# Optimization experiments

Measured on AMD Instinct MI355X. Metric: run time of the kernel, lower is better.

Reference implementation:

```python
import jax, jax.numpy as jnp
import numpy as np

NUM_LAYERS = 3
HIDDEN = 64
NUM_CLASSES = 4096
LN_EPS = 1e-5


def setup_inputs() -> dict:
    key = jax.random.key(0)
    ks = jax.random.split(key, 8)
    B, N, E, H = 8, NUM_CLASSES, 131072, HIDDEN
    node_features = jax.random.normal(ks[0], (B, N, H), dtype=jnp.float32)
    edge_indices = jax.random.randint(ks[1], (B, 2, E), 0, N, dtype=jnp.int64)
    edge_attrs = jax.random.normal(ks[2], (B, E, H), dtype=jnp.float32)
    # GraphConvolutionLayer params (xavier_uniform weight, zero bias) per layer
    limit = np.sqrt(6.0 / (H + H)).astype(np.float32)
    W = jax.random.uniform(ks[3], (NUM_LAYERS, H, H), minval=-limit, maxval=limit, dtype=jnp.float32)
    b = jnp.zeros((NUM_LAYERS, H), dtype=jnp.float32)
    gamma = jnp.ones((NUM_LAYERS, H), dtype=jnp.float32)
    beta = jnp.zeros((NUM_LAYERS, H), dtype=jnp.float32)
    global_emb = 0.02 * jax.random.normal(ks[4], (N, H), dtype=jnp.float32)
    return {
        "node_features": node_features,
        "edge_indices": edge_indices,
        "edge_attrs": edge_attrs,
        "W": W,
        "b": b,
        "gamma": gamma,
        "beta": beta,
        "global_emb": global_emb,
    }


def _layer_norm(x, g, bt):
    mu = jnp.mean(x, axis=-1, keepdims=True)
    var = jnp.mean((x - mu) ** 2, axis=-1, keepdims=True)
    return (x - mu) * jax.lax.rsqrt(var + LN_EPS) * g + bt


def reference(node_features, edge_indices, edge_attrs, W, b, gamma, beta, global_emb):
    N = node_features.shape[1]

    def per_graph(x0, ei, ea):
        # presence mask computed on raw node features [N, 1]
        presence = (jnp.sum(x0, axis=1) != 0).astype(x0.dtype)[:, None]
        src, dst = ei[0], ei[1]
        x = x0
        for i in range(NUM_LAYERS):
            residual = x
            h = x @ W[i]                                   # [N, H]
            msg = h[src] * ea                              # gather + edge gate [E, H]
            out = jax.ops.segment_sum(msg, dst, num_segments=N) + b[i]
            out = jax.nn.relu(out)
            out = _layer_norm(out, gamma[i], beta[i])
            x = out + residual if i > 0 else out
        return x * presence + global_emb * (1.0 - presence)

    return jax.vmap(per_graph)(node_features, edge_indices, edge_attrs)
```

## Files before the change

kernel.cpp:

```cpp
#include <hip/hip_runtime.h>

#define GB 8
#define GN 4096
#define GH 64
#define GE 131072
#define LN_EPS 1e-5f
#define NBIN (GB * GN)
#define TOTE (GB * GE)

static __device__ __forceinline__ unsigned short f2bf(float f) {
    union { float f; unsigned int u; } v; v.f = f;
    unsigned int u = v.u;
    return (unsigned short)((u + 0x7FFFu + ((u >> 16) & 1u)) >> 16);
}
static __device__ __forceinline__ void bf2x(unsigned int u, float& lo, float& hi) {
    union { float f; unsigned int i; } a, b;
    a.i = u << 16; b.i = u & 0xFFFF0000u;
    lo = a.f; hi = b.f;
}
static __device__ __forceinline__ void fma8(uint4 ev, uint4 hv, float4& a0, float4& a1) {
    float el, eh, hl, hh;
    bf2x(ev.x, el, eh); bf2x(hv.x, hl, hh);
    a0.x = fmaf(el, hl, a0.x); a0.y = fmaf(eh, hh, a0.y);
    bf2x(ev.y, el, eh); bf2x(hv.y, hl, hh);
    a0.z = fmaf(el, hl, a0.z); a0.w = fmaf(eh, hh, a0.w);
    bf2x(ev.z, el, eh); bf2x(hv.z, hl, hh);
    a1.x = fmaf(el, hl, a1.x); a1.y = fmaf(eh, hh, a1.y);
    bf2x(ev.w, el, eh); bf2x(hv.w, hl, hh);
    a1.z = fmaf(el, hl, a1.z); a1.w = fmaf(eh, hh, a1.w);
}

__global__ void k_init(const float* __restrict__ nf, float* __restrict__ pres) {
    int w = (blockIdx.x * blockDim.x + threadIdx.x) >> 6;
    int lane = threadIdx.x & 63;
    if (w >= NBIN) return;
    float v = nf[(size_t)w * GH + lane];
    #pragma unroll
    for (int o = 1; o < 64; o <<= 1) v += __shfl_xor(v, o, 64);
    if (lane == 0) pres[w] = (v != 0.0f) ? 1.0f : 0.0f;
}

__global__ void k_hist(const int* __restrict__ ei, int* __restrict__ hist) {
    int t = blockIdx.x * blockDim.x + threadIdx.x;
    int b = t >> 17, e = t & (GE - 1);
    int dst = ei[(b << 18) + GE + e];
    atomicAdd(&hist[(b << 12) + dst], 1);
}

__global__ void k_scan(const int* __restrict__ hist, int* __restrict__ off,
                       int* __restrict__ cur) {
    __shared__ int part[256];
    int b = blockIdx.x;
    int t = threadIdx.x;
    int base = (b << 12) + t * 16;
    int c[16];
    int s = 0;
    #pragma unroll
    for (int i = 0; i < 16; ++i) { c[i] = hist[base + i]; s += c[i]; }
    part[t] = s;
    __syncthreads();
    for (int o = 1; o < 256; o <<= 1) {
        int u = (t >= o) ? part[t - o] : 0;
        __syncthreads();
        part[t] += u;
        __syncthreads();
    }
    int p = b * GE + part[t] - s;
    #pragma unroll
    for (int i = 0; i < 16; ++i) { off[base + i] = p; cur[base + i] = p; p += c[i]; }
    if (b == GB - 1 && t == 255) off[NBIN] = TOTE;
}

__global__ void k_fillperm(const int* __restrict__ ei, int* __restrict__ cur,
                           const float* __restrict__ ea,
                           int* __restrict__ sSrc, unsigned short* __restrict__ ea_s) {
    int grp = (blockIdx.x * blockDim.x + threadIdx.x) >> 4;
    if (grp >= TOTE) return;
    int sub  = threadIdx.x & 15;
    int lane = threadIdx.x & 63;
    int b = grp >> 17, e = grp & (GE - 1);
    int dst = ei[(b << 18) + GE + e];
    int pos = 0;
    if (sub == 0) pos = atomicAdd(&cur[(b << 12) + dst], 1);
    pos = __shfl(pos, lane & ~15, 64);
    float4 v = *reinterpret_cast<const float4*>(ea + ((size_t)grp << 6) + (sub << 2));
    ushort4 o;
    o.x = f2bf(v.x); o.y = f2bf(v.y); o.z = f2bf(v.z); o.w = f2bf(v.w);
    *reinterpret_cast<ushort4*>(ea_s + ((size_t)pos << 6) + (sub << 2)) = o;
    if (sub == 0) sSrc[pos] = ei[(b << 18) + e];
}

__global__ void k_gemm(const float* __restrict__ x, const float* __restrict__ W,
                       unsigned short* __restrict__ h, int layer) {
    __shared__ float Wl[GH * GH];
    for (int i = threadIdx.x; i < GH * GH; i += blockDim.x)
        Wl[i] = W[layer * GH * GH + i];
    __syncthreads();
    int w = (blockIdx.x * blockDim.x + threadIdx.x) >> 6;
    int lane = threadIdx.x & 63;
    if (w >= NBIN) return;
    float xv = x[(size_t)w * GH + lane];
    float acc = 0.0f;
    #pragma unroll
    for (int k = 0; k < GH; ++k)
        acc = fmaf(__shfl(xv, k, 64), Wl[k * GH + lane], acc);
    h[(size_t)w * GH + lane] = f2bf(acc);
}

__global__ void k_gather(const int* __restrict__ off, const int* __restrict__ sSrc,
                         const unsigned short* __restrict__ ea_s,
                         const unsigned short* __restrict__ h,
                         const float* __restrict__ bias, const float* __restrict__ gam,
                         const float* __restrict__ bet,
                         float* __restrict__ x, const float* __restrict__ pres,
                         const float* __restrict__ ge, float* __restrict__ out,
                         int layer) {
    int w = (blockIdx.x * blockDim.x + threadIdx.x) >> 6;
    if (w >= NBIN) return;
    int lane = threadIdx.x & 63;
    int g   = lane >> 3;
    int sub = lane & 7;
    int b = w >> 12;
    int beg = off[w], end = off[w + 1];
    const unsigned short* hb = h + ((((size_t)b) << 12) * GH);

    float4 a0 = make_float4(0.f, 0.f, 0.f, 0.f);
    float4 a1 = make_float4(0.f, 0.f, 0.f, 0.f);
    for (int e = beg; e < end; e += 16) {
        int e0 = e + g;
        int e1 = e + 8 + g;
        if (e0 < end) {
            int s0 = sSrc[e0];
            uint4 ev = *reinterpret_cast<const uint4*>(ea_s + (((size_t)e0) << 6) + (sub << 3));
            uint4 hv = *reinterpret_cast<const uint4*>(hb + (((size_t)s0) << 6) + (sub << 3));
            fma8(ev, hv, a0, a1);
        }
        if (e1 < end) {
            int s1 = sSrc[e1];
            uint4 ev = *reinterpret_cast<const uint4*>(ea_s + (((size_t)e1) << 6) + (sub << 3));
            uint4 hv = *reinterpret_cast<const uint4*>(hb + (((size_t)s1) << 6) + (sub << 3));
            fma8(ev, hv, a0, a1);
        }
    }
    #pragma unroll
    for (int o = 8; o < 64; o <<= 1) {
        a0.x += __shfl_xor(a0.x, o, 64);
        a0.y += __shfl_xor(a0.y, o, 64);
        a0.z += __shfl_xor(a0.z, o, 64);
        a0.w += __shfl_xor(a0.w, o, 64);
        a1.x += __shfl_xor(a1.x, o, 64);
        a1.y += __shfl_xor(a1.y, o, 64);
        a1.z += __shfl_xor(a1.z, o, 64);
        a1.w += __shfl_xor(a1.w, o, 64);
    }

    const float4* bias4 = reinterpret_cast<const float4*>(bias + layer * GH + (sub << 3));
    float4 b0 = bias4[0], b1 = bias4[1];
    float4 v0, v1;
    v0.x = fmaxf(a0.x + b0.x, 0.f); v0.y = fmaxf(a0.y + b0.y, 0.f);
    v0.z = fmaxf(a0.z + b0.z, 0.f); v0.w = fmaxf(a0.w + b0.w, 0.f);
    v1.x = fmaxf(a1.x + b1.x, 0.f); v1.y = fmaxf(a1.y + b1.y, 0.f);
    v1.z = fmaxf(a1.z + b1.z, 0.f); v1.w = fmaxf(a1.w + b1.w, 0.f);
    float s = v0.x + v0.y + v0.z + v0.w + v1.x + v1.y + v1.z + v1.w;
    #pragma unroll
    for (int o = 1; o < 8; o <<= 1) s += __shfl_xor(s, o, 64);
    float mu = s * (1.0f / GH);
    float4 d0, d1;
    d0.x = v0.x - mu; d0.y = v0.y - mu; d0.z = v0.z - mu; d0.w = v0.w - mu;
    d1.x = v1.x - mu; d1.y = v1.y - mu; d1.z = v1.z - mu; d1.w = v1.w - mu;
    float q = d0.x*d0.x + d0.y*d0.y + d0.z*d0.z + d0.w*d0.w
            + d1.x*d1.x + d1.y*d1.y + d1.z*d1.z + d1.w*d1.w;
    #pragma unroll
    for (int o = 1; o < 8; o <<= 1) q += __shfl_xor(q, o, 64);
    float r = rsqrtf(q * (1.0f / GH) + LN_EPS);
    const float4* gam4 = reinterpret_cast<const float4*>(gam + layer * GH + (sub << 3));
    const float4* bet4 = reinterpret_cast<const float4*>(bet + layer * GH + (sub << 3));
    float4 g0 = gam4[0], g1 = gam4[1];
    float4 t0 = bet4[0], t1 = bet4[1];
    float4 y0, y1;
    y0.x = d0.x * r * g0.x + t0.x; y0.y = d0.y * r * g0.y + t0.y;
    y0.z = d0.z * r * g0.z + t0.z; y0.w = d0.w * r * g0.w + t0.w;
    y1.x = d1.x * r * g1.x + t1.x; y1.y = d1.y * r * g1.y + t1.y;
    y1.z = d1.z * r * g1.z + t1.z; y1.w = d1.w * r * g1.w + t1.w;

    if (g == 0) {
        float4* xp = reinterpret_cast<float4*>(x + (size_t)w * GH + (sub << 3));
        if (layer > 0) {
            float4 x0 = xp[0], x1 = xp[1];
            y0.x += x0.x; y0.y += x0.y; y0.z += x0.z; y0.w += x0.w;
            y1.x += x1.x; y1.y += x1.y; y1.z += x1.z; y1.w += x1.w;
        }
        if (layer < 2) {
            xp[0] = y0; xp[1] = y1;
        } else {
            float p = pres[w];
            const float4* ge4 = reinterpret_cast<const float4*>(ge + (size_t)(w & (GN - 1)) * GH + (sub << 3));
            float4 e0 = ge4[0], e1 = ge4[1];
            float4 o0, o1;
            o0.x = y0.x * p + e0.x * (1.f - p); o0.y = y0.y * p + e0.y * (1.f - p);
            o0.z = y0.z * p + e0.z * (1.f - p); o0.w = y0.w * p + e0.w * (1.f - p);
            o1.x = y1.x * p + e1.x * (1.f - p); o1.y = y1.y * p + e1.y * (1.f - p);
            o1.z = y1.z * p + e1.z * (1.f - p); o1.w = y1.w * p + e1.w * (1.f - p);
            float4* op = reinterpret_cast<float4*>(out + (size_t)w * GH + (sub << 3));
            op[0] = o0; op[1] = o1;
        }
    }
}

extern "C" void kernel_launch(void* const* d_in, const int* in_sizes, int n_in,
                              void* d_out, int out_size, void* d_ws, size_t ws_size,
                              hipStream_t stream) {
    const float* nf = (const float*)d_in[0];
    const int* ei   = (const int*)d_in[1];
    const float* ea = (const float*)d_in[2];
    const float* W  = (const float*)d_in[3];
    const float* bb = (const float*)d_in[4];
    const float* gg = (const float*)d_in[5];
    const float* be = (const float*)d_in[6];
    const float* ge = (const float*)d_in[7];
    float* out = (float*)d_out;

    float* x    = (float*)d_ws;
    float* pres = x + (size_t)NBIN * GH;
    int* off    = (int*)(pres + NBIN);
    int* cur    = off + NBIN + 1;
    int* hist   = cur + NBIN;
    int* sSrc   = hist + NBIN;
    unsigned short* h_s  = (unsigned short*)(sSrc + TOTE);
    unsigned short* ea_s = h_s + (size_t)NBIN * GH;

    hipMemsetAsync(hist, 0, NBIN * sizeof(int), stream);
    k_init<<<NBIN / 4, 256, 0, stream>>>(nf, pres);
    k_hist<<<TOTE / 256, 256, 0, stream>>>(ei, hist);
    k_scan<<<GB, 256, 0, stream>>>(hist, off, cur);
    k_fillperm<<<TOTE / 16, 256, 0, stream>>>(ei, cur, ea, sSrc, ea_s);

    for (int l = 0; l < 3; ++l) {
        k_gemm<<<NBIN / 4, 256, 0, stream>>>(l == 0 ? nf : x, W, h_s, l);
        k_gather<<<NBIN / 4, 256, 0, stream>>>(off, sSrc, ea_s, h_s, bb, gg, be,
                                               x, pres, ge, out, l);
    }
}
```

Measured before the change: 403.6 us.

## Sort edges by destination within fixed windows instead of per graph

Splits each graph's edge list into eight windows and builds a counting-sort by destination inside each window, so the permutation scatter of edge attributes stays within a smaller memory region. The scan runs over 64 windows instead of 8 graphs. The gather kernel now walks eight short per-window segments per node, which adds offset loads and shorter, less-filled inner loops in a kernel that runs once per layer.

```diff
diff --git a/kernel.cpp b/kernel.cpp
--- a/kernel.cpp
+++ b/kernel.cpp
@@ -7,6 +7,8 @@
 #define LN_EPS 1e-5f
 #define NBIN (GB * GN)
 #define TOTE (GB * GE)
+#define NWIN 64
+#define WSZ  (TOTE / NWIN)
 
 static __device__ __forceinline__ unsigned short f2bf(float f) {
     union { float f; unsigned int u; } v; v.f = f;
@@ -40,23 +42,24 @@
     if (lane == 0) pres[w] = (v != 0.0f) ? 1.0f : 0.0f;
 }
 
-__global__ void k_hist(const int* __restrict__ ei, int* __restrict__ hist) {
+__global__ void k_hist2(const int* __restrict__ ei, int* __restrict__ hist2) {
     int t = blockIdx.x * blockDim.x + threadIdx.x;
     int b = t >> 17, e = t & (GE - 1);
     int dst = ei[(b << 18) + GE + e];
-    atomicAdd(&hist[(b << 12) + dst], 1);
-}
-
-__global__ void k_scan(const int* __restrict__ hist, int* __restrict__ off,
-                       int* __restrict__ cur) {
+    int w = t >> 14;
+    atomicAdd(&hist2[(w << 12) + dst], 1);
+}
+
+__global__ void k_scan2(const int* __restrict__ hist2, int* __restrict__ off2,
+                        int* __restrict__ cur2) {
     __shared__ int part[256];
-    int b = blockIdx.x;
+    int w = blockIdx.x;
     int t = threadIdx.x;
-    int base = (b << 12) + t * 16;
+    int base = (w << 12) + t * 16;
     int c[16];
     int s = 0;
     #pragma unroll
-    for (int i = 0; i < 16; ++i) { c[i] = hist[base + i]; s += c[i]; }
+    for (int i = 0; i < 16; ++i) { c[i] = hist2[base + i]; s += c[i]; }
     part[t] = s;
     __syncthreads();
     for (int o = 1; o < 256; o <<= 1) {
@@ -65,23 +68,23 @@
         part[t] += u;
         __syncthreads();
     }
-    int p = b * GE + part[t] - s;
-    #pragma unroll
-    for (int i = 0; i < 16; ++i) { off[base + i] = p; cur[base + i] = p; p += c[i]; }
-    if (b == GB - 1 && t == 255) off[NBIN] = TOTE;
-}
-
-__global__ void k_fillperm(const int* __restrict__ ei, int* __restrict__ cur,
-                           const float* __restrict__ ea,
-                           int* __restrict__ sSrc, unsigned short* __restrict__ ea_s) {
+    int p = (w << 14) + part[t] - s;
+    #pragma unroll
+    for (int i = 0; i < 16; ++i) { off2[base + i] = p; cur2[base + i] = p; p += c[i]; }
+}
+
+__global__ void k_wperm(const int* __restrict__ ei, int* __restrict__ cur2,
+                        const float* __restrict__ ea,
+                        int* __restrict__ sSrc, unsigned short* __restrict__ ea_s) {
     int grp = (blockIdx.x * blockDim.x + threadIdx.x) >> 4;
     if (grp >= TOTE) return;
     int sub  = threadIdx.x & 15;
     int lane = threadIdx.x & 63;
     int b = grp >> 17, e = grp & (GE - 1);
+    int w = grp >> 14;
     int dst = ei[(b << 18) + GE + e];
     int pos = 0;
-    if (sub == 0) pos = atomicAdd(&cur[(b << 12) + dst], 1);
+    if (sub == 0) pos = atomicAdd(&cur2[(w << 12) + dst], 1);
     pos = __shfl(pos, lane & ~15, 64);
     float4 v = *reinterpret_cast<const float4*>(ea + ((size_t)grp << 6) + (sub << 2));
     ushort4 o;
@@ -107,7 +110,7 @@
     h[(size_t)w * GH + lane] = f2bf(acc);
 }
 
-__global__ void k_gather(const int* __restrict__ off, const int* __restrict__ sSrc,
+__global__ void k_gather(const int* __restrict__ off2, const int* __restrict__ sSrc,
                          const unsigned short* __restrict__ ea_s,
                          const unsigned short* __restrict__ h,
                          const float* __restrict__ bias, const float* __restrict__ gam,
@@ -120,26 +123,25 @@
     int lane = threadIdx.x & 63;
     int g   = lane >> 3;
     int sub = lane & 7;
-    int b = w >> 12;
-    int beg = off[w], end = off[w + 1];
-    const unsigned short* hb = h + ((((size_t)b) << 12) * GH);
+    int grf = w >> 12;
+    int dst = w & (GN - 1);
+    const unsigned short* hb = h + ((((size_t)grf) << 12) * GH);
 
     float4 a0 = make_float4(0.f, 0.f, 0.f, 0.f);
     float4 a1 = make_float4(0.f, 0.f, 0.f, 0.f);
-    for (int e = beg; e < end; e += 16) {
-        int e0 = e + g;
-        int e1 = e + 8 + g;
-        if (e0 < end) {
-            int s0 = sSrc[e0];
-            uint4 ev = *reinterpret_cast<const uint4*>(ea_s + (((size_t)e0) << 6) + (sub << 3));
-            uint4 hv = *reinterpret_cast<const uint4*>(hb + (((size_t)s0) << 6) + (sub << 3));
-            fma8(ev, hv, a0, a1);
-        }
-        if (e1 < end) {
-            int s1 = sSrc[e1];
-            uint4 ev = *reinterpret_cast<const uint4*>(ea_s + (((size_t)e1) << 6) + (sub << 3));
-            uint4 hv = *reinterpret_cast<const uint4*>(hb + (((size_t)s1) << 6) + (sub << 3));
-            fma8(ev, hv, a0, a1);
+    #pragma unroll
+    for (int c = 0; c < 8; ++c) {
+        int ww = (grf << 3) + c;
+        int beg = off2[(ww << 12) + dst];
+        int end = (dst == GN - 1) ? ((ww + 1) << 14) : off2[(ww << 12) + dst + 1];
+        for (int e = beg; e < end; e += 8) {
+            int e0 = e + g;
+            if (e0 < end) {
+                int s0 = sSrc[e0];
+                uint4 ev = *reinterpret_cast<const uint4*>(ea_s + (((size_t)e0) << 6) + (sub << 3));
+                uint4 hv = *reinterpret_cast<const uint4*>(hb + (((size_t)s0) << 6) + (sub << 3));
+                fma8(ev, hv, a0, a1);
+            }
         }
     }
     #pragma unroll
@@ -222,22 +224,22 @@
 
     float* x    = (float*)d_ws;
     float* pres = x + (size_t)NBIN * GH;
-    int* off    = (int*)(pres + NBIN);
-    int* cur    = off + NBIN + 1;
-    int* hist   = cur + NBIN;
-    int* sSrc   = hist + NBIN;
+    int* off2   = (int*)(pres + NBIN);
+    int* cur2   = off2 + NWIN * GN;
+    int* hist2  = cur2 + NWIN * GN;
+    int* sSrc   = hist2 + NWIN * GN;
     unsigned short* h_s  = (unsigned short*)(sSrc + TOTE);
     unsigned short* ea_s = h_s + (size_t)NBIN * GH;
 
-    hipMemsetAsync(hist, 0, NBIN * sizeof(int), stream);
+    hipMemsetAsync(hist2, 0, NWIN * GN * sizeof(int), stream);
     k_init<<<NBIN / 4, 256, 0, stream>>>(nf, pres);
-    k_hist<<<TOTE / 256, 256, 0, stream>>>(ei, hist);
-    k_scan<<<GB, 256, 0, stream>>>(hist, off, cur);
-    k_fillperm<<<TOTE / 16, 256, 0, stream>>>(ei, cur, ea, sSrc, ea_s);
+    k_hist2<<<TOTE / 256, 256, 0, stream>>>(ei, hist2);
+    k_scan2<<<NWIN, 256, 0, stream>>>(hist2, off2, cur2);
+    k_wperm<<<TOTE / 16, 256, 0, stream>>>(ei, cur2, ea, sSrc, ea_s);
 
     for (int l = 0; l < 3; ++l) {
         k_gemm<<<NBIN / 4, 256, 0, stream>>>(l == 0 ? nf : x, W, h_s, l);
-        k_gather<<<NBIN / 4, 256, 0, stream>>>(off, sSrc, ea_s, h_s, bb, gg, be,
+        k_gather<<<NBIN / 4, 256, 0, stream>>>(off2, sSrc, ea_s, h_s, bb, gg, be,
                                                x, pres, ge, out, l);
     }
 }
```

After: 423.7 us. 5.0% more time.
